# Optimization experiments

Hardware: AMD Instinct MI355X
Metric: run time of the kernel (lower is better)

## Reference

```python
import jax, jax.numpy as jnp
import numpy as np

BINS = 64
LAMBDA_AFFINE = 1.0
LAMBDA_SIM = 1.0
EPS = 1e-10

B, C, D, H, W = 2, 1, 192, 224, 192


def setup_inputs() -> dict:
    key = jax.random.key(0)
    k1, k2, k3, k4 = jax.random.split(key, 4)
    return {
        "predicted_affine": jax.random.normal(k1, (B, 12), dtype=jnp.float32),
        "true_affine": jax.random.normal(k2, (B, 12), dtype=jnp.float32),
        "fixed": jax.random.uniform(k3, (B, C, D, H, W), dtype=jnp.float32),
        "warped": jax.random.uniform(k4, (B, C, D, H, W), dtype=jnp.float32),
    }


def _bin_indices(x_flat):
    # x_flat: (B, N) -> int32 bin indices in [0, BINS-1]
    xmin = x_flat.min(axis=1, keepdims=True)
    xmax = x_flat.max(axis=1, keepdims=True)
    norm = (x_flat - xmin) / (xmax - xmin + EPS) * (BINS - 1)
    return jnp.clip(norm.astype(jnp.int32), 0, BINS - 1)


def mutual_information(fixed, warped):
    # take first channel, flatten per sample
    f = fixed[:, 0].reshape(fixed.shape[0], -1)   # (B, N)
    w = warped[:, 0].reshape(warped.shape[0], -1)  # (B, N)
    b = f.shape[0]
    fi = _bin_indices(f)
    wi = _bin_indices(w)
    # joint histogram per batch via one fused scatter-add (segment_sum)
    batch_off = (jnp.arange(b, dtype=jnp.int32) * (BINS * BINS))[:, None]
    flat_idx = (batch_off + fi * BINS + wi).reshape(-1)
    counts = jax.ops.segment_sum(
        jnp.ones(flat_idx.shape, dtype=jnp.float32), flat_idx,
        num_segments=b * BINS * BINS)
    joint = counts.reshape(b, BINS, BINS)
    joint = joint / (joint.sum(axis=(1, 2), keepdims=True) + EPS)
    p_f = joint.sum(axis=2)  # (B, BINS)
    p_w = joint.sum(axis=1)  # (B, BINS)
    h_f = -jnp.sum(p_f * jnp.log(p_f + EPS), axis=1)
    h_w = -jnp.sum(p_w * jnp.log(p_w + EPS), axis=1)
    h_j = -jnp.sum(joint * jnp.log(joint + EPS), axis=(1, 2))
    mi = h_f + h_w - h_j
    nmi = 2.0 * mi / (h_f + h_w + EPS)  # normalized=True
    return -nmi.mean()


def reference(predicted_affine, true_affine, fixed, warped):
    affine_loss = jnp.mean((predicted_affine - true_affine) ** 2)
    similarity_loss = mutual_information(fixed, warped)
    total_loss = LAMBDA_AFFINE * affine_loss + LAMBDA_SIM * similarity_loss
    return total_loss
```

## Files before the change

kernel.cpp:

```cpp
#include <hip/hip_runtime.h>
#include <cfloat>
#include <math.h>

#define BINS 64
#define NELEM (192*224*192)
#define NB 2
#define HIST_OFF 16

__device__ __forceinline__ unsigned fkey(float f){
    unsigned u = __float_as_uint(f);
    return (u & 0x80000000u) ? ~u : (u | 0x80000000u);
}
__device__ __forceinline__ float funkey(unsigned k){
    unsigned u = (k & 0x80000000u) ? (k ^ 0x80000000u) : ~k;
    return __uint_as_float(u);
}

__global__ void k_init(unsigned* ws){
    int i = blockIdx.x * 256 + threadIdx.x;
    if (i < 16) ws[i] = ((i & 1) == 0) ? 0xFFFFFFFFu : 0u;
    if (i < NB * BINS * BINS) ws[HIST_OFF + i] = 0u;
}

__global__ void k_minmax(const float* __restrict__ F, const float* __restrict__ W,
                         unsigned* ws){
    const int b = blockIdx.y;
    const float4* F4 = (const float4*)(F + (size_t)b * NELEM);
    const float4* W4 = (const float4*)(W + (size_t)b * NELEM);
    const int n4 = NELEM / 4;
    float fmn = FLT_MAX, fmx = -FLT_MAX, wmn = FLT_MAX, wmx = -FLT_MAX;
    for (int i = blockIdx.x * blockDim.x + threadIdx.x; i < n4;
         i += gridDim.x * blockDim.x){
        float4 a = F4[i], c = W4[i];
        fmn = fminf(fmn, fminf(fminf(a.x, a.y), fminf(a.z, a.w)));
        fmx = fmaxf(fmx, fmaxf(fmaxf(a.x, a.y), fmaxf(a.z, a.w)));
        wmn = fminf(wmn, fminf(fminf(c.x, c.y), fminf(c.z, c.w)));
        wmx = fmaxf(wmx, fmaxf(fmaxf(c.x, c.y), fmaxf(c.z, c.w)));
    }
    for (int off = 32; off; off >>= 1){
        fmn = fminf(fmn, __shfl_down(fmn, off));
        fmx = fmaxf(fmx, __shfl_down(fmx, off));
        wmn = fminf(wmn, __shfl_down(wmn, off));
        wmx = fmaxf(wmx, __shfl_down(wmx, off));
    }
    __shared__ float s[4][4];
    int wave = threadIdx.x >> 6;
    if ((threadIdx.x & 63) == 0){
        s[wave][0] = fmn; s[wave][1] = fmx; s[wave][2] = wmn; s[wave][3] = wmx;
    }
    __syncthreads();
    if (threadIdx.x == 0){
        float a0 = s[0][0], a1 = s[0][1], a2 = s[0][2], a3 = s[0][3];
        for (int wv = 1; wv < 4; ++wv){
            a0 = fminf(a0, s[wv][0]); a1 = fmaxf(a1, s[wv][1]);
            a2 = fminf(a2, s[wv][2]); a3 = fmaxf(a3, s[wv][3]);
        }
        atomicMin(&ws[b*4+0], fkey(a0));
        atomicMax(&ws[b*4+1], fkey(a1));
        atomicMin(&ws[b*4+2], fkey(a2));
        atomicMax(&ws[b*4+3], fkey(a3));
    }
}

__global__ void k_hist(const float* __restrict__ F, const float* __restrict__ W,
                       unsigned* ws){
    const int b = blockIdx.y;
    __shared__ unsigned h[BINS * BINS];
    for (int i = threadIdx.x; i < BINS * BINS; i += blockDim.x) h[i] = 0u;
    __syncthreads();
    const float fmn = funkey(ws[b*4+0]);
    const float fmx = funkey(ws[b*4+1]);
    const float wmn = funkey(ws[b*4+2]);
    const float wmx = funkey(ws[b*4+3]);
    const float fden = fmx - fmn + 1e-10f;
    const float wden = wmx - wmn + 1e-10f;
    const float4* F4 = (const float4*)(F + (size_t)b * NELEM);
    const float4* W4 = (const float4*)(W + (size_t)b * NELEM);
    const int n4 = NELEM / 4;
    for (int i = blockIdx.x * blockDim.x + threadIdx.x; i < n4;
         i += gridDim.x * blockDim.x){
        float4 a = F4[i], c = W4[i];
        float fa[4] = {a.x, a.y, a.z, a.w};
        float wa[4] = {c.x, c.y, c.z, c.w};
        #pragma unroll
        for (int k = 0; k < 4; ++k){
            int fi = (int)((fa[k] - fmn) / fden * 63.0f);
            int wi = (int)((wa[k] - wmn) / wden * 63.0f);
            fi = min(max(fi, 0), 63);
            wi = min(max(wi, 0), 63);
            atomicAdd(&h[fi * BINS + wi], 1u);
        }
    }
    __syncthreads();
    unsigned* gh = ws + HIST_OFF + b * BINS * BINS;
    for (int i = threadIdx.x; i < BINS * BINS; i += blockDim.x){
        unsigned v = h[i];
        if (v) atomicAdd(&gh[i], v);
    }
}

__device__ double block_sum256(double v, double* sred){
    int t = threadIdx.x;
    sred[t] = v; __syncthreads();
    for (int off = 128; off; off >>= 1){
        if (t < off) sred[t] += sred[t + off];
        __syncthreads();
    }
    double r = sred[0]; __syncthreads();
    return r;
}

__global__ void k_final(const float* __restrict__ pa, const float* __restrict__ ta,
                        const unsigned* __restrict__ ws, float* __restrict__ out){
    __shared__ double sred[256];
    const unsigned* hist = ws + HIST_OFF;
    const double invN = 1.0 / (double)NELEM;
    double loss_sim = 0.0;
    for (int b = 0; b < NB; ++b){
        const unsigned* H = hist + b * BINS * BINS;
        double hj_p = 0.0;
        for (int i = threadIdx.x; i < BINS * BINS; i += 256){
            double p = (double)H[i] * invN;
            hj_p += p * log(p + 1e-10);
        }
        double hj = -block_sum256(hj_p, sred);
        double hf_p = 0.0, hw_p = 0.0;
        if (threadIdx.x < BINS){
            int r = threadIdx.x;
            double pf = 0.0, pw = 0.0;
            for (int j = 0; j < BINS; ++j){
                pf += (double)H[r * BINS + j];
                pw += (double)H[j * BINS + r];
            }
            pf *= invN; pw *= invN;
            hf_p = pf * log(pf + 1e-10);
            hw_p = pw * log(pw + 1e-10);
        }
        double hf = -block_sum256(hf_p, sred);
        double hw = -block_sum256(hw_p, sred);
        double mi  = hf + hw - hj;
        double nmi = 2.0 * mi / (hf + hw + 1e-10);
        loss_sim += -nmi;
    }
    loss_sim /= (double)NB;
    if (threadIdx.x == 0){
        double a = 0.0;
        for (int i = 0; i < 24; ++i){
            double d = (double)pa[i] - (double)ta[i];
            a += d * d;
        }
        a /= 24.0;
        out[0] = (float)(a + loss_sim);
    }
}

extern "C" void kernel_launch(void* const* d_in, const int* in_sizes, int n_in,
                              void* d_out, int out_size, void* d_ws, size_t ws_size,
                              hipStream_t stream) {
    const float* pa = (const float*)d_in[0];
    const float* ta = (const float*)d_in[1];
    const float* F  = (const float*)d_in[2];
    const float* W  = (const float*)d_in[3];
    float* out = (float*)d_out;
    unsigned* ws = (unsigned*)d_ws;

    k_init<<<dim3(32 + 1), 256, 0, stream>>>(ws);
    k_minmax<<<dim3(512, NB), 256, 0, stream>>>(F, W, ws);
    k_hist<<<dim3(256, NB), 256, 0, stream>>>(F, W, ws);
    k_final<<<1, 256, 0, stream>>>(pa, ta, ws, out);
}
```

Baseline: 242.4 us.

## Enlarge grids, unroll loads two-deep, replace divides with reciprocal scale

```diff
diff --git a/kernel.cpp b/kernel.cpp
--- a/kernel.cpp
+++ b/kernel.cpp
@@ -4,8 +4,11 @@
 
 #define BINS 64
 #define NELEM (192*224*192)
+#define N4    (NELEM/4)
 #define NB 2
 #define HIST_OFF 16
+#define BLK 256
+#define GBLK 1024
 
 __device__ __forceinline__ unsigned fkey(float f){
     unsigned u = __float_as_uint(f);
@@ -22,21 +25,33 @@
     if (i < NB * BINS * BINS) ws[HIST_OFF + i] = 0u;
 }
 
-__global__ void k_minmax(const float* __restrict__ F, const float* __restrict__ W,
-                         unsigned* ws){
+__device__ __forceinline__ void mm4(const float4& v, float& mn, float& mx){
+    mn = fminf(mn, fminf(fminf(v.x, v.y), fminf(v.z, v.w)));
+    mx = fmaxf(mx, fmaxf(fmaxf(v.x, v.y), fmaxf(v.z, v.w)));
+}
+
+__global__ __launch_bounds__(BLK) void k_minmax(const float* __restrict__ F,
+                                                const float* __restrict__ W,
+                                                unsigned* ws){
     const int b = blockIdx.y;
     const float4* F4 = (const float4*)(F + (size_t)b * NELEM);
     const float4* W4 = (const float4*)(W + (size_t)b * NELEM);
-    const int n4 = NELEM / 4;
+    const int stride = GBLK * BLK;
     float fmn = FLT_MAX, fmx = -FLT_MAX, wmn = FLT_MAX, wmx = -FLT_MAX;
-    for (int i = blockIdx.x * blockDim.x + threadIdx.x; i < n4;
-         i += gridDim.x * blockDim.x){
-        float4 a = F4[i], c = W4[i];
-        fmn = fminf(fmn, fminf(fminf(a.x, a.y), fminf(a.z, a.w)));
-        fmx = fmaxf(fmx, fmaxf(fmaxf(a.x, a.y), fmaxf(a.z, a.w)));
-        wmn = fminf(wmn, fminf(fminf(c.x, c.y), fminf(c.z, c.w)));
-        wmx = fmaxf(wmx, fmaxf(fmaxf(c.x, c.y), fmaxf(c.z, c.w)));
-    }
+
+    int i = blockIdx.x * BLK + threadIdx.x;
+    while (i + stride < N4){
+        float4 a0 = F4[i], c0 = W4[i];
+        float4 a1 = F4[i + stride], c1 = W4[i + stride];
+        mm4(a0, fmn, fmx); mm4(a1, fmn, fmx);
+        mm4(c0, wmn, wmx); mm4(c1, wmn, wmx);
+        i += 2 * stride;
+    }
+    if (i < N4){
+        float4 a0 = F4[i], c0 = W4[i];
+        mm4(a0, fmn, fmx); mm4(c0, wmn, wmx);
+    }
+
     for (int off = 32; off; off >>= 1){
         fmn = fminf(fmn, __shfl_down(fmn, off));
         fmx = fmaxf(fmx, __shfl_down(fmx, off));
@@ -62,40 +77,58 @@
     }
 }
 
-__global__ void k_hist(const float* __restrict__ F, const float* __restrict__ W,
-                       unsigned* ws){
+__device__ __forceinline__ void bin4(const float4& fa, const float4& wa,
+                                     float fmn, float wmn, float fsc, float wsc,
+                                     unsigned* h){
+    float fv[4] = {fa.x, fa.y, fa.z, fa.w};
+    float wv[4] = {wa.x, wa.y, wa.z, wa.w};
+    #pragma unroll
+    for (int j = 0; j < 4; ++j){
+        int fi = (int)((fv[j] - fmn) * fsc);
+        int wi = (int)((wv[j] - wmn) * wsc);
+        fi = min(max(fi, 0), 63);
+        wi = min(max(wi, 0), 63);
+        atomicAdd(&h[fi * BINS + wi], 1u);
+    }
+}
+
+__global__ __launch_bounds__(BLK) void k_hist(const float* __restrict__ F,
+                                              const float* __restrict__ W,
+                                              unsigned* ws){
     const int b = blockIdx.y;
     __shared__ unsigned h[BINS * BINS];
-    for (int i = threadIdx.x; i < BINS * BINS; i += blockDim.x) h[i] = 0u;
-    __syncthreads();
+    for (int i = threadIdx.x; i < BINS * BINS; i += BLK) h[i] = 0u;
+
     const float fmn = funkey(ws[b*4+0]);
     const float fmx = funkey(ws[b*4+1]);
     const float wmn = funkey(ws[b*4+2]);
     const float wmx = funkey(ws[b*4+3]);
-    const float fden = fmx - fmn + 1e-10f;
-    const float wden = wmx - wmn + 1e-10f;
+    const float fsc = 63.0f / (fmx - fmn + 1e-10f);
+    const float wsc = 63.0f / (wmx - wmn + 1e-10f);
+
     const float4* F4 = (const float4*)(F + (size_t)b * NELEM);
     const float4* W4 = (const float4*)(W + (size_t)b * NELEM);
-    const int n4 = NELEM / 4;
-    for (int i = blockIdx.x * blockDim.x + threadIdx.x; i < n4;
-         i += gridDim.x * blockDim.x){
-        float4 a = F4[i], c = W4[i];
-        float fa[4] = {a.x, a.y, a.z, a.w};
-        float wa[4] = {c.x, c.y, c.z, c.w};
-        #pragma unroll
-        for (int k = 0; k < 4; ++k){
-            int fi = (int)((fa[k] - fmn) / fden * 63.0f);
-            int wi = (int)((wa[k] - wmn) / wden * 63.0f);
-            fi = min(max(fi, 0), 63);
-            wi = min(max(wi, 0), 63);
-            atomicAdd(&h[fi * BINS + wi], 1u);
-        }
-    }
+    const int stride = GBLK * BLK;
+    __syncthreads();
+
+    int i = blockIdx.x * BLK + threadIdx.x;
+    while (i + stride < N4){
+        float4 a0 = F4[i], c0 = W4[i];
+        float4 a1 = F4[i + stride], c1 = W4[i + stride];
+        bin4(a0, c0, fmn, wmn, fsc, wsc, h);
+        bin4(a1, c1, fmn, wmn, fsc, wsc, h);
+        i += 2 * stride;
+    }
+    if (i < N4){
+        float4 a0 = F4[i], c0 = W4[i];
+        bin4(a0, c0, fmn, wmn, fsc, wsc, h);
+    }
+
     __syncthreads();
     unsigned* gh = ws + HIST_OFF + b * BINS * BINS;
-    for (int i = threadIdx.x; i < BINS * BINS; i += blockDim.x){
-        unsigned v = h[i];
-        if (v) atomicAdd(&gh[i], v);
+    for (int i2 = threadIdx.x; i2 < BINS * BINS; i2 += BLK){
+        unsigned v = h[i2];
+        if (v) atomicAdd(&gh[i2], v);
     }
 }
 
@@ -114,27 +147,27 @@
                         const unsigned* __restrict__ ws, float* __restrict__ out){
     __shared__ double sred[256];
     const unsigned* hist = ws + HIST_OFF;
-    const double invN = 1.0 / (double)NELEM;
+    const float fN = (float)NELEM;
     double loss_sim = 0.0;
     for (int b = 0; b < NB; ++b){
         const unsigned* H = hist + b * BINS * BINS;
         double hj_p = 0.0;
         for (int i = threadIdx.x; i < BINS * BINS; i += 256){
-            double p = (double)H[i] * invN;
-            hj_p += p * log(p + 1e-10);
+            float p = (float)H[i] / fN;
+            hj_p += (double)(p * logf(p + 1e-10f));
         }
         double hj = -block_sum256(hj_p, sred);
         double hf_p = 0.0, hw_p = 0.0;
         if (threadIdx.x < BINS){
             int r = threadIdx.x;
-            double pf = 0.0, pw = 0.0;
+            unsigned cf = 0, cw = 0;
             for (int j = 0; j < BINS; ++j){
-                pf += (double)H[r * BINS + j];
-                pw += (double)H[j * BINS + r];
+                cf += H[r * BINS + j];
+                cw += H[j * BINS + r];
             }
-            pf *= invN; pw *= invN;
-            hf_p = pf * log(pf + 1e-10);
-            hw_p = pw * log(pw + 1e-10);
+            float pf = (float)cf / fN, pw = (float)cw / fN;
+            hf_p = (double)(pf * logf(pf + 1e-10f));
+            hw_p = (double)(pw * logf(pw + 1e-10f));
         }
         double hf = -block_sum256(hf_p, sred);
         double hw = -block_sum256(hw_p, sred);
@@ -164,8 +197,8 @@
     float* out = (float*)d_out;
     unsigned* ws = (unsigned*)d_ws;
 
-    k_init<<<dim3(32 + 1), 256, 0, stream>>>(ws);
-    k_minmax<<<dim3(512, NB), 256, 0, stream>>>(F, W, ws);
-    k_hist<<<dim3(256, NB), 256, 0, stream>>>(F, W, ws);
+    k_init<<<33, 256, 0, stream>>>(ws);
+    k_minmax<<<dim3(GBLK, NB), BLK, 0, stream>>>(F, W, ws);
+    k_hist<<<dim3(GBLK, NB), BLK, 0, stream>>>(F, W, ws);
     k_final<<<1, 256, 0, stream>>>(pa, ta, ws, out);
 }
```

New measurement: 287.7 us. 18.7% more time.
